# Performance work log

Hardware: AMD Instinct MI355X
Metric: run time of the kernel (lower is better)

## Reference

```python
import jax, jax.numpy as jnp
import numpy as np

LAMDA = 0.05
TAU = 0.44
MARGIN = 0.05
PD_EPS = 1e-6   # torch F.pairwise_distance default eps
NORM_EPS = 1e-12  # torch F.normalize default eps

B, C = 131072, 256


def setup_inputs() -> dict:
    key = jax.random.key(0)
    k1, k2 = jax.random.split(key)
    inputs = jax.random.normal(k1, (B, C), dtype=jnp.float32)
    labels = jax.random.randint(k2, (B,), 0, C, dtype=jnp.int64)
    return {"inputs": inputs, "labels": labels}


def _hinge_loss(inputs, labels):
    # F.normalize along dim=1: x / max(||x||_2, eps)
    nrm = jnp.sqrt(jnp.sum(inputs * inputs, axis=1, keepdims=True))
    x = inputs / jnp.maximum(nrm, NORM_EPS)
    a, b = x[0::2], x[1::2]            # [B/2, C] each pair (idx, idx+1)
    # F.pairwise_distance(x,y)^2 = sum((x - y + eps)^2)
    d2 = jnp.sum((a - b + PD_EPS) ** 2, axis=1)  # [B/2]
    eq = labels[0::2] == labels[1::2]
    # Faithful to original: l starts at -1 and is STICKY once set to +1
    # (original code never resets l after a matching pair).
    l = jnp.where(jnp.cumsum(eq.astype(jnp.int32)) > 0, 1.0, -1.0)
    loss_hinge = jnp.sum(jax.nn.relu(MARGIN - l * (TAU - d2)))
    return loss_hinge  # scalar (mean of 0-d tensor == itself)


def reference(inputs, labels):
    # cross entropy with mean reduction
    logp = jax.nn.log_softmax(inputs, axis=-1)
    ce = -jnp.mean(jnp.take_along_axis(logp, labels[:, None], axis=1))
    return ce + LAMDA * _hinge_loss(inputs, labels) / 2.0
```

## Files before the change

kernel.cpp:

```cpp
#include <hip/hip_runtime.h>
#include <cstddef>

#define NROWS 131072
#define NCOLS 256
#define NPAIRS 65536
#define PBLK 256
#define PWAVES 4
#define PITER 2
#define PAIRS_PER_WAVE (4 * PITER)
#define NBLK (NPAIRS / (PWAVES * PAIRS_PER_WAVE))
#define GBLK 256


__device__ __forceinline__ float rsum16(float x) {
    x += __int_as_float(__builtin_amdgcn_update_dpp(0, __float_as_int(x), 0x121, 0xF, 0xF, false));
    x += __int_as_float(__builtin_amdgcn_update_dpp(0, __float_as_int(x), 0x122, 0xF, 0xF, false));
    x += __int_as_float(__builtin_amdgcn_update_dpp(0, __float_as_int(x), 0x124, 0xF, 0xF, false));
    x += __int_as_float(__builtin_amdgcn_update_dpp(0, __float_as_int(x), 0x128, 0xF, 0xF, false));
    return x;
}

__device__ __forceinline__ float dpp_sum(float x) {
    x = rsum16(x);
    x += __int_as_float(__builtin_amdgcn_update_dpp(0, __float_as_int(x), 0x142, 0xA, 0xF, false));
    x += __int_as_float(__builtin_amdgcn_update_dpp(0, __float_as_int(x), 0x143, 0xC, 0xF, false));
    return x;
}

__device__ __forceinline__ unsigned dpp_umin(unsigned x) {
    unsigned y;
    y = (unsigned)__builtin_amdgcn_update_dpp((int)x, (int)x, 0x121, 0xF, 0xF, false); x = x < y ? x : y;
    y = (unsigned)__builtin_amdgcn_update_dpp((int)x, (int)x, 0x122, 0xF, 0xF, false); x = x < y ? x : y;
    y = (unsigned)__builtin_amdgcn_update_dpp((int)x, (int)x, 0x124, 0xF, 0xF, false); x = x < y ? x : y;
    y = (unsigned)__builtin_amdgcn_update_dpp((int)x, (int)x, 0x128, 0xF, 0xF, false); x = x < y ? x : y;
    y = (unsigned)__builtin_amdgcn_update_dpp((int)x, (int)x, 0x142, 0xA, 0xF, false); x = x < y ? x : y;
    y = (unsigned)__builtin_amdgcn_update_dpp((int)x, (int)x, 0x143, 0xC, 0xF, false); x = x < y ? x : y;
    return x;
}

__global__ __launch_bounds__(256) void dcnn_gp0(
    const float* __restrict__ in, const int* __restrict__ labels,
    unsigned* __restrict__ minslot, float* __restrict__ ceg)
{
    const int p = blockIdx.x * 256 + threadIdx.x;
    int2 L = reinterpret_cast<const int2*>(labels)[p];
    float va = in[(size_t)(2 * p) * NCOLS + L.x];
    float vb = in[(size_t)(2 * p + 1) * NCOLS + L.y];
    float g = va + vb;
    unsigned m = (L.x == L.y) ? (unsigned)p : 0xFFFFFFFFu;
    g = dpp_sum(g);
    m = dpp_umin(m);
    __shared__ float gs[4];
    __shared__ unsigned ms[4];
    const int lane = threadIdx.x & 63, w = threadIdx.x >> 6;
    if (lane == 63) { gs[w] = g; ms[w] = m; }
    __syncthreads();
    if (threadIdx.x == 0) {
        ceg[blockIdx.x] = (gs[0] + gs[1]) + (gs[2] + gs[3]);
        unsigned a = ms[0] < ms[1] ? ms[0] : ms[1];
        unsigned b = ms[2] < ms[3] ? ms[2] : ms[3];
        minslot[blockIdx.x] = a < b ? a : b;
    }
}

__global__ __launch_bounds__(PBLK) void dcnn_pair(
    const float* __restrict__ in,
    const unsigned* __restrict__ minslot,
    float* __restrict__ lse_blk, float* __restrict__ h_blk)
{
    const int wave = threadIdx.x >> 6;
    const int lane = threadIdx.x & 63;
    const int g = lane >> 4;
    const int s = lane & 15;

    unsigned m0 = minslot[lane], m1 = minslot[lane + 64];
    unsigned m2 = minslot[lane + 128], m3 = minslot[lane + 192];
    unsigned mm = m0 < m1 ? m0 : m1;
    unsigned mn = m2 < m3 ? m2 : m3;
    mm = mm < mn ? mm : mn;
    unsigned p0 = (unsigned)__builtin_amdgcn_readlane((int)dpp_umin(mm), 63);

    const int wbase = (blockIdx.x * PWAVES + wave) * PAIRS_PER_WAVE;
    float lse_acc = 0.0f, h_acc = 0.0f;

    #pragma unroll
    for (int it = 0; it < PITER; ++it) {
        const int P = wbase + it * 4 + g;
        const float* rowa = in + (size_t)(2 * P) * NCOLS + 4 * s;
        const float* rowb = rowa + NCOLS;
        float4 a0 = *(const float4*)(rowa);
        float4 b0 = *(const float4*)(rowb);
        float4 a1 = *(const float4*)(rowa + 64);
        float4 b1 = *(const float4*)(rowb + 64);
        float4 a2 = *(const float4*)(rowa + 128);
        float4 b2 = *(const float4*)(rowb + 128);
        float4 a3 = *(const float4*)(rowa + 192);
        float4 b3 = *(const float4*)(rowb + 192);

        float ea0 = (__expf(a0.x) + __expf(a0.y)) + (__expf(a0.z) + __expf(a0.w));
        float ea1 = (__expf(a1.x) + __expf(a1.y)) + (__expf(a1.z) + __expf(a1.w));
        float ea2 = (__expf(a2.x) + __expf(a2.y)) + (__expf(a2.z) + __expf(a2.w));
        float ea3 = (__expf(a3.x) + __expf(a3.y)) + (__expf(a3.z) + __expf(a3.w));
        float se_a = (ea0 + ea1) + (ea2 + ea3);
        float eb0 = (__expf(b0.x) + __expf(b0.y)) + (__expf(b0.z) + __expf(b0.w));
        float eb1 = (__expf(b1.x) + __expf(b1.y)) + (__expf(b1.z) + __expf(b1.w));
        float eb2 = (__expf(b2.x) + __expf(b2.y)) + (__expf(b2.z) + __expf(b2.w));
        float eb3 = (__expf(b3.x) + __expf(b3.y)) + (__expf(b3.z) + __expf(b3.w));
        float se_b = (eb0 + eb1) + (eb2 + eb3);

        float sa0 = fmaf(a0.x, a0.x, fmaf(a0.y, a0.y, fmaf(a0.z, a0.z, a0.w * a0.w)));
        float sa1 = fmaf(a1.x, a1.x, fmaf(a1.y, a1.y, fmaf(a1.z, a1.z, a1.w * a1.w)));
        float sa2 = fmaf(a2.x, a2.x, fmaf(a2.y, a2.y, fmaf(a2.z, a2.z, a2.w * a2.w)));
        float sa3 = fmaf(a3.x, a3.x, fmaf(a3.y, a3.y, fmaf(a3.z, a3.z, a3.w * a3.w)));
        float ssa = (sa0 + sa1) + (sa2 + sa3);
        float sb0 = fmaf(b0.x, b0.x, fmaf(b0.y, b0.y, fmaf(b0.z, b0.z, b0.w * b0.w)));
        float sb1 = fmaf(b1.x, b1.x, fmaf(b1.y, b1.y, fmaf(b1.z, b1.z, b1.w * b1.w)));
        float sb2 = fmaf(b2.x, b2.x, fmaf(b2.y, b2.y, fmaf(b2.z, b2.z, b2.w * b2.w)));
        float sb3 = fmaf(b3.x, b3.x, fmaf(b3.y, b3.y, fmaf(b3.z, b3.z, b3.w * b3.w)));
        float ssb = (sb0 + sb1) + (sb2 + sb3);
        float dt0 = fmaf(a0.x, b0.x, fmaf(a0.y, b0.y, fmaf(a0.z, b0.z, a0.w * b0.w)));
        float dt1 = fmaf(a1.x, b1.x, fmaf(a1.y, b1.y, fmaf(a1.z, b1.z, a1.w * b1.w)));
        float dt2 = fmaf(a2.x, b2.x, fmaf(a2.y, b2.y, fmaf(a2.z, b2.z, a2.w * b2.w)));
        float dt3 = fmaf(a3.x, b3.x, fmaf(a3.y, b3.y, fmaf(a3.z, b3.z, a3.w * b3.w)));
        float dot = (dt0 + dt1) + (dt2 + dt3);

        se_a = rsum16(se_a);
        se_b = rsum16(se_b);
        ssa = rsum16(ssa);
        ssb = rsum16(ssb);
        dot = rsum16(dot);

        if (s == 0) {
            lse_acc += __logf(se_a) + __logf(se_b);
            float inva = rsqrtf(ssa);
            float invb = rsqrtf(ssb);
            float d2 = 2.0f + 2.56e-10f - 2.0f * dot * inva * invb;
            float l = ((unsigned)P >= p0) ? 1.0f : -1.0f;
            h_acc += fmaxf(0.05f - l * (0.44f - d2), 0.0f);
        }
    }

    __shared__ float lw[PWAVES * 4], hw[PWAVES * 4];
    if (s == 0) { lw[wave * 4 + g] = lse_acc; hw[wave * 4 + g] = h_acc; }
    __syncthreads();
    if (threadIdx.x == 0) {
        float c = 0.0f, h = 0.0f;
        #pragma unroll
        for (int i = 0; i < PWAVES * 4; ++i) { c += lw[i]; h += hw[i]; }
        lse_blk[blockIdx.x] = c;
        h_blk[blockIdx.x] = h;
    }
}

__global__ __launch_bounds__(1024) void dcnn_final(
    const float* __restrict__ lse_blk, const float* __restrict__ h_blk,
    const float* __restrict__ ceg, float* __restrict__ out)
{
    const int t = threadIdx.x;
    float c = lse_blk[t] + lse_blk[t + 1024];
    float h = h_blk[t] + h_blk[t + 1024];
    float gv = (t < GBLK) ? ceg[t] : 0.0f;
    c = dpp_sum(c);
    h = dpp_sum(h);
    gv = dpp_sum(gv);
    __shared__ float cs[16], hs[16], gs[16];
    if ((t & 63) == 63) { cs[t >> 6] = c; hs[t >> 6] = h; gs[t >> 6] = gv; }
    __syncthreads();
    if (t == 0) {
        float C = 0.0f, H = 0.0f, G = 0.0f;
        #pragma unroll
        for (int i = 0; i < 16; ++i) { C += cs[i]; H += hs[i]; G += gs[i]; }
        out[0] = (C - G) * (1.0f / (float)NROWS) + 0.025f * H;
    }
}

extern "C" void kernel_launch(void* const* d_in, const int* in_sizes, int n_in,
                              void* d_out, int out_size, void* d_ws, size_t ws_size,
                              hipStream_t stream) {
    const float* in = (const float*)d_in[0];
    const int* labels = (const int*)d_in[1];
    float* wsf = (float*)d_ws;
    unsigned* minslot = (unsigned*)d_ws;
    float* ceg = wsf + 256;
    float* lse_blk = wsf + 512;
    float* h_blk = wsf + 512 + NBLK;
    float* out = (float*)d_out;

    dcnn_gp0<<<GBLK, 256, 0, stream>>>(in, labels, minslot, ceg);
    dcnn_pair<<<NBLK, PBLK, 0, stream>>>(in, minslot, lse_blk, h_blk);
    dcnn_final<<<1, 1024, 0, stream>>>(lse_blk, h_blk, ceg, out);
}
```

Measured before the change: 195.7 us.

## Fuse label gather and min-pair scan into main pass, defer hinge to final

Measured after the change: 195.8 us. About the same (+0.0%).

```diff
diff --git a/kernel.cpp b/kernel.cpp
--- a/kernel.cpp
+++ b/kernel.cpp
@@ -8,8 +8,8 @@
 #define PWAVES 4
 #define PITER 2
 #define PAIRS_PER_WAVE (4 * PITER)
-#define NBLK (NPAIRS / (PWAVES * PAIRS_PER_WAVE))
-#define GBLK 256
+#define PAIRS_PER_BLOCK (PWAVES * PAIRS_PER_WAVE)
+#define NBLK (NPAIRS / PAIRS_PER_BLOCK)
 
 
 __device__ __forceinline__ float rsum16(float x) {
@@ -38,50 +38,19 @@
     return x;
 }
 
-__global__ __launch_bounds__(256) void dcnn_gp0(
+__global__ __launch_bounds__(PBLK) void dcnn_main(
     const float* __restrict__ in, const int* __restrict__ labels,
-    unsigned* __restrict__ minslot, float* __restrict__ ceg)
-{
-    const int p = blockIdx.x * 256 + threadIdx.x;
-    int2 L = reinterpret_cast<const int2*>(labels)[p];
-    float va = in[(size_t)(2 * p) * NCOLS + L.x];
-    float vb = in[(size_t)(2 * p + 1) * NCOLS + L.y];
-    float g = va + vb;
-    unsigned m = (L.x == L.y) ? (unsigned)p : 0xFFFFFFFFu;
-    g = dpp_sum(g);
-    m = dpp_umin(m);
-    __shared__ float gs[4];
-    __shared__ unsigned ms[4];
-    const int lane = threadIdx.x & 63, w = threadIdx.x >> 6;
-    if (lane == 63) { gs[w] = g; ms[w] = m; }
-    __syncthreads();
-    if (threadIdx.x == 0) {
-        ceg[blockIdx.x] = (gs[0] + gs[1]) + (gs[2] + gs[3]);
-        unsigned a = ms[0] < ms[1] ? ms[0] : ms[1];
-        unsigned b = ms[2] < ms[3] ? ms[2] : ms[3];
-        minslot[blockIdx.x] = a < b ? a : b;
-    }
-}
-
-__global__ __launch_bounds__(PBLK) void dcnn_pair(
-    const float* __restrict__ in,
-    const unsigned* __restrict__ minslot,
-    float* __restrict__ lse_blk, float* __restrict__ h_blk)
+    unsigned* __restrict__ min_blk, float* __restrict__ ce_blk,
+    float* __restrict__ d2arr)
 {
     const int wave = threadIdx.x >> 6;
     const int lane = threadIdx.x & 63;
     const int g = lane >> 4;
     const int s = lane & 15;
-
-    unsigned m0 = minslot[lane], m1 = minslot[lane + 64];
-    unsigned m2 = minslot[lane + 128], m3 = minslot[lane + 192];
-    unsigned mm = m0 < m1 ? m0 : m1;
-    unsigned mn = m2 < m3 ? m2 : m3;
-    mm = mm < mn ? mm : mn;
-    unsigned p0 = (unsigned)__builtin_amdgcn_readlane((int)dpp_umin(mm), 63);
-
     const int wbase = (blockIdx.x * PWAVES + wave) * PAIRS_PER_WAVE;
-    float lse_acc = 0.0f, h_acc = 0.0f;
+
+    float ce_acc = 0.0f;
+    unsigned mcand = 0xFFFFFFFFu;
 
     #pragma unroll
     for (int it = 0; it < PITER; ++it) {
@@ -96,6 +65,7 @@
         float4 b2 = *(const float4*)(rowb + 128);
         float4 a3 = *(const float4*)(rowa + 192);
         float4 b3 = *(const float4*)(rowb + 192);
+        int2 L = *(const int2*)(labels + 2 * P);
 
         float ea0 = (__expf(a0.x) + __expf(a0.y)) + (__expf(a0.z) + __expf(a0.w));
         float ea1 = (__expf(a1.x) + __expf(a1.y)) + (__expf(a1.z) + __expf(a1.w));
@@ -124,6 +94,21 @@
         float dt3 = fmaf(a3.x, b3.x, fmaf(a3.y, b3.y, fmaf(a3.z, b3.z, a3.w * b3.w)));
         float dot = (dt0 + dt1) + (dt2 + dt3);
 
+        {
+            int c = L.x;
+            if (((c >> 2) & 15) == s) {
+                int i = c >> 6, k = c & 3;
+                float4 r = i == 0 ? a0 : i == 1 ? a1 : i == 2 ? a2 : a3;
+                ce_acc -= (k == 0 ? r.x : k == 1 ? r.y : k == 2 ? r.z : r.w);
+            }
+            c = L.y;
+            if (((c >> 2) & 15) == s) {
+                int i = c >> 6, k = c & 3;
+                float4 r = i == 0 ? b0 : i == 1 ? b1 : i == 2 ? b2 : b3;
+                ce_acc -= (k == 0 ? r.x : k == 1 ? r.y : k == 2 ? r.z : r.w);
+            }
+        }
+
         se_a = rsum16(se_a);
         se_b = rsum16(se_b);
         ssa = rsum16(ssa);
@@ -131,46 +116,78 @@
         dot = rsum16(dot);
 
         if (s == 0) {
-            lse_acc += __logf(se_a) + __logf(se_b);
+            ce_acc += __logf(se_a) + __logf(se_b);
             float inva = rsqrtf(ssa);
             float invb = rsqrtf(ssb);
             float d2 = 2.0f + 2.56e-10f - 2.0f * dot * inva * invb;
-            float l = ((unsigned)P >= p0) ? 1.0f : -1.0f;
-            h_acc += fmaxf(0.05f - l * (0.44f - d2), 0.0f);
+            d2arr[P] = d2;
+            if (L.x == L.y) mcand = mcand < (unsigned)P ? mcand : (unsigned)P;
         }
     }
 
-    __shared__ float lw[PWAVES * 4], hw[PWAVES * 4];
-    if (s == 0) { lw[wave * 4 + g] = lse_acc; hw[wave * 4 + g] = h_acc; }
+    ce_acc = dpp_sum(ce_acc);
+    mcand = dpp_umin(mcand);
+    __shared__ float cw[PWAVES];
+    __shared__ unsigned mw[PWAVES];
+    if (lane == 63) { cw[wave] = ce_acc; mw[wave] = mcand; }
     __syncthreads();
     if (threadIdx.x == 0) {
-        float c = 0.0f, h = 0.0f;
-        #pragma unroll
-        for (int i = 0; i < PWAVES * 4; ++i) { c += lw[i]; h += hw[i]; }
-        lse_blk[blockIdx.x] = c;
-        h_blk[blockIdx.x] = h;
+        ce_blk[blockIdx.x] = (cw[0] + cw[1]) + (cw[2] + cw[3]);
+        unsigned m01 = mw[0] < mw[1] ? mw[0] : mw[1];
+        unsigned m23 = mw[2] < mw[3] ? mw[2] : mw[3];
+        min_blk[blockIdx.x] = m01 < m23 ? m01 : m23;
     }
 }
 
 __global__ __launch_bounds__(1024) void dcnn_final(
-    const float* __restrict__ lse_blk, const float* __restrict__ h_blk,
-    const float* __restrict__ ceg, float* __restrict__ out)
+    const unsigned* __restrict__ min_blk, const float* __restrict__ ce_blk,
+    const float* __restrict__ d2arr, float* __restrict__ out)
 {
     const int t = threadIdx.x;
-    float c = lse_blk[t] + lse_blk[t + 1024];
-    float h = h_blk[t] + h_blk[t + 1024];
-    float gv = (t < GBLK) ? ceg[t] : 0.0f;
+    const int lane = t & 63, w = t >> 6;
+    __shared__ unsigned msh[16];
+    __shared__ float csh[16], hsh[16];
+    __shared__ unsigned p0sh;
+
+    unsigned m0 = min_blk[t], m1 = min_blk[t + 1024];
+    unsigned m = m0 < m1 ? m0 : m1;
+    m = dpp_umin(m);
+    if (lane == 63) msh[w] = m;
+    __syncthreads();
+    if (t == 0) {
+        unsigned mm = msh[0];
+        #pragma unroll
+        for (int i = 1; i < 16; ++i) mm = mm < msh[i] ? mm : msh[i];
+        p0sh = mm;
+    }
+    __syncthreads();
+    const unsigned p0 = p0sh;
+
+    float c = ce_blk[t] + ce_blk[t + 1024];
+
+    const float4* d4 = reinterpret_cast<const float4*>(d2arr);
+    float h = 0.0f;
+    #pragma unroll
+    for (int j = 0; j < 16; ++j) {
+        int idx = t + 1024 * j;
+        float4 d = d4[idx];
+        unsigned Pb = (unsigned)(idx * 4);
+        float l;
+        l = (Pb + 0 >= p0) ? 1.0f : -1.0f; h += fmaxf(0.05f - l * (0.44f - d.x), 0.0f);
+        l = (Pb + 1 >= p0) ? 1.0f : -1.0f; h += fmaxf(0.05f - l * (0.44f - d.y), 0.0f);
+        l = (Pb + 2 >= p0) ? 1.0f : -1.0f; h += fmaxf(0.05f - l * (0.44f - d.z), 0.0f);
+        l = (Pb + 3 >= p0) ? 1.0f : -1.0f; h += fmaxf(0.05f - l * (0.44f - d.w), 0.0f);
+    }
+
     c = dpp_sum(c);
     h = dpp_sum(h);
-    gv = dpp_sum(gv);
-    __shared__ float cs[16], hs[16], gs[16];
-    if ((t & 63) == 63) { cs[t >> 6] = c; hs[t >> 6] = h; gs[t >> 6] = gv; }
+    if (lane == 63) { csh[w] = c; hsh[w] = h; }
     __syncthreads();
     if (t == 0) {
-        float C = 0.0f, H = 0.0f, G = 0.0f;
+        float C = 0.0f, H = 0.0f;
         #pragma unroll
-        for (int i = 0; i < 16; ++i) { C += cs[i]; H += hs[i]; G += gs[i]; }
-        out[0] = (C - G) * (1.0f / (float)NROWS) + 0.025f * H;
+        for (int i = 0; i < 16; ++i) { C += csh[i]; H += hsh[i]; }
+        out[0] = C * (1.0f / (float)NROWS) + 0.025f * H;
     }
 }
 
@@ -179,14 +196,11 @@
                               hipStream_t stream) {
     const float* in = (const float*)d_in[0];
     const int* labels = (const int*)d_in[1];
-    float* wsf = (float*)d_ws;
-    unsigned* minslot = (unsigned*)d_ws;
-    float* ceg = wsf + 256;
-    float* lse_blk = wsf + 512;
-    float* h_blk = wsf + 512 + NBLK;
+    unsigned* min_blk = (unsigned*)d_ws;
+    float* ce_blk = (float*)d_ws + NBLK;
+    float* d2arr = (float*)d_ws + 2 * NBLK;
     float* out = (float*)d_out;
 
-    dcnn_gp0<<<GBLK, 256, 0, stream>>>(in, labels, minslot, ceg);
-    dcnn_pair<<<NBLK, PBLK, 0, stream>>>(in, minslot, lse_blk, h_blk);
-    dcnn_final<<<1, 1024, 0, stream>>>(lse_blk, h_blk, ceg, out);
-}
+    dcnn_main<<<NBLK, PBLK, 0, stream>>>(in, labels, min_blk, ce_blk, d2arr);
+    dcnn_final<<<1, 1024, 0, stream>>>(min_blk, ce_blk, d2arr, out);
+}
```
